# Kernel tuning notes

Hardware: AMD Instinct MI355X
Metric: run time of the kernel (lower is better)

The kernel has to match this reference:

```python
import jax, jax.numpy as jnp
import numpy as np

B, N, C, H = 4, 2048, 1024, 16
D = C // H  # head_dim = 64

def setup_inputs() -> dict:
    key = jax.random.key(0)
    k1, k2, k3, k4, k5, k6 = jax.random.split(key, 6)
    x = jax.random.normal(k1, (B, N, C), dtype=jnp.float32)
    rope_cos = jax.random.uniform(k2, (N, D), dtype=jnp.float32)
    rope_sin = jax.random.uniform(k3, (N, D), dtype=jnp.float32)
    w_qkv = jax.random.normal(k4, (3 * C, C), dtype=jnp.float32) * (C ** -0.5)
    w_proj = jax.random.normal(k5, (C, C), dtype=jnp.float32) * (C ** -0.5)
    b_proj = jax.random.normal(k6, (C,), dtype=jnp.float32) * 0.01
    return {"x": x, "rope_cos": rope_cos, "rope_sin": rope_sin,
            "w_qkv": w_qkv, "w_proj": w_proj, "b_proj": b_proj}

def _rotate_half(x):
    x1, x2 = jnp.split(x, 2, axis=-1)
    return jnp.concatenate((-x2, x1), axis=-1)

def _apply_rope(x, cos, sin):
    # x: [B,H,N,D]; cos/sin: [N,D] broadcast over B,H
    return x * cos + _rotate_half(x) * sin

def reference(x, rope_cos, rope_sin, w_qkv, w_proj, b_proj):
    Bc, Nc, Cc = x.shape
    scale = D ** -0.5
    qkv = jnp.einsum('bnc,fc->bnf', x, w_qkv)            # [B,N,3C]
    qkv = qkv.reshape(Bc, Nc, 3, H, D).transpose(2, 0, 3, 1, 4)  # [3,B,H,N,D]
    q, k, v = qkv[0], qkv[1], qkv[2]
    q = _apply_rope(q, rope_cos, rope_sin)
    k = _apply_rope(k, rope_cos, rope_sin)
    attn = jnp.einsum('bhnd,bhmd->bhnm', q, k) * scale   # [B,H,N,N]
    attn = jax.nn.softmax(attn, axis=-1)
    out = jnp.einsum('bhnm,bhmd->bhnd', attn, v)         # [B,H,N,D]
    out = out.transpose(0, 2, 1, 3).reshape(Bc, Nc, Cc)  # [B,N,C]
    return jnp.einsum('bnc,fc->bnf', out, w_proj) + b_proj
```

## Files before the change

### kernel.cpp

```cpp
#include <hip/hip_runtime.h>

#define MM   8192
#define CC   1024
#define F3   3072
#define NN   2048
#define HH   16
#define DD   64
#define QSCALE 0.1803368801111731f

typedef __attribute__((ext_vector_type(8))) __bf16 bf16x8;
typedef __attribute__((ext_vector_type(4))) float floatx4;
typedef __attribute__((ext_vector_type(4))) unsigned uintx4;

__device__ __forceinline__ unsigned short f2b(float f) {
  union { float f; unsigned int u; } v; v.f = f;
  unsigned int r = v.u + 0x7fffu + ((v.u >> 16) & 1u);
  return (unsigned short)(r >> 16);
}
__device__ __forceinline__ float b2f(unsigned short b) {
  union { unsigned int u; float f; } v; v.u = ((unsigned int)b) << 16;
  return v.f;
}

__device__ __forceinline__ void gl_lds16(const unsigned short* g, unsigned short* l) {
  __builtin_amdgcn_global_load_lds((const __attribute__((address_space(1))) void*)g,
                                   (__attribute__((address_space(3))) void*)l, 16, 0, 0);
}

__global__ __launch_bounds__(256) void cvt_all_k(const float* __restrict__ x,
                                                 const float* __restrict__ wqkv,
                                                 const float* __restrict__ wproj,
                                                 unsigned short* __restrict__ xb,
                                                 unsigned short* __restrict__ wqkvb,
                                                 unsigned short* __restrict__ wprojb) {
  const int N0 = MM * CC / 4, N1 = F3 * CC / 4, N2 = CC * CC / 4;
  const int total = N0 + N1 + N2;
  const int stride = (int)gridDim.x * 256;
  for (int i = blockIdx.x * 256 + threadIdx.x; i < total; i += stride) {
    const float* src;
    unsigned short* dst;
    int j;
    if (i < N0)            { src = x;     dst = xb;     j = i; }
    else if (i < N0 + N1)  { src = wqkv;  dst = wqkvb;  j = i - N0; }
    else                   { src = wproj; dst = wprojb; j = i - N0 - N1; }
    float4 v = ((const float4*)src)[j];
    ushort4 o;
    o.x = f2b(v.x); o.y = f2b(v.y); o.z = f2b(v.z); o.w = f2b(v.w);
    ((ushort4*)dst)[j] = o;
  }
}

template <int F, bool BF16OUT, bool ROPE>
__global__ __launch_bounds__(512, 2) void gemm_p(const unsigned short* __restrict__ A,
                                                 const unsigned short* __restrict__ Bm,
                                                 void* __restrict__ Cout,
                                                 const float* __restrict__ bias,
                                                 const float* __restrict__ rcp,
                                                 const float* __restrict__ spp, int K) {
  __shared__ alignas(16) unsigned short lA[3][128 * 64];
  __shared__ alignas(16) unsigned short lB[3][256 * 64];
  const int tid = threadIdx.x, lane = tid & 63, wave = tid >> 6;
  const int r16 = lane & 15, q4 = lane >> 4;
  const int wm = wave & 1, wn = wave >> 1;

  const int id = blockIdx.x;
  const int xcd = id & 7, slot = id >> 3;
  const int rx = xcd * 8 + (slot & 7), cy = slot >> 3;
  const int rowBase = rx * 128, colBase = cy * 256;

  const int cA0 = tid, cA1 = tid + 512;
  const int cB0 = tid, cB1 = tid + 512, cB2 = tid + 1024, cB3 = tid + 1536;
#define CHOFF(base, c) ((size_t)((base) + ((c) >> 3)) * K + ((((c) & 7) ^ (((c) >> 3) & 7)) << 3))
  const size_t aoff0 = CHOFF(rowBase, cA0), aoff1 = CHOFF(rowBase, cA1);
  const size_t boff0 = CHOFF(colBase, cB0), boff1 = CHOFF(colBase, cB1);
  const size_t boff2 = CHOFF(colBase, cB2), boff3 = CHOFF(colBase, cB3);
#undef CHOFF

#define STAGEP(kt, bsel) do { const int _k0 = (kt) * 64; \
    gl_lds16(A + aoff0 + _k0, &lA[bsel][cA0 * 8]); \
    gl_lds16(A + aoff1 + _k0, &lA[bsel][cA1 * 8]); \
    gl_lds16(Bm + boff0 + _k0, &lB[bsel][cB0 * 8]); \
    gl_lds16(Bm + boff1 + _k0, &lB[bsel][cB1 * 8]); \
    gl_lds16(Bm + boff2 + _k0, &lB[bsel][cB2 * 8]); \
    gl_lds16(Bm + boff3 + _k0, &lB[bsel][cB3 * 8]); } while (0)

  floatx4 acc[4][4];
  const floatx4 z = {0.f, 0.f, 0.f, 0.f};
#pragma unroll
  for (int i = 0; i < 4; ++i)
#pragma unroll
    for (int j = 0; j < 4; ++j) acc[i][j] = z;

  const int nt = K / 64;

  STAGEP(0, 0);
  STAGEP(1, 1);
  STAGEP(2, 2);
  asm volatile("s_waitcnt vmcnt(12)" ::: "memory");
  __builtin_amdgcn_s_barrier();
  __builtin_amdgcn_sched_barrier(0);

  int bs = 0;
  for (int t = 0; t < nt; ++t) {
    const unsigned short* la = &lA[bs][0];
    const unsigned short* lb = &lB[bs][0];
    bf16x8 af[4][2], bv[4][2];
#pragma unroll
    for (int im = 0; im < 4; ++im) {
      int row = wm * 64 + im * 16 + r16, r7 = row & 7;
      af[im][0] = *(const bf16x8*)(la + row * 64 + ((q4 ^ r7) << 3));
      af[im][1] = *(const bf16x8*)(la + row * 64 + (((4 + q4) ^ r7) << 3));
    }
#pragma unroll
    for (int jf = 0; jf < 4; ++jf) {
      int row = wn * 64 + jf * 16 + r16, r7 = row & 7;
      bv[jf][0] = *(const bf16x8*)(lb + row * 64 + ((q4 ^ r7) << 3));
      bv[jf][1] = *(const bf16x8*)(lb + row * 64 + (((4 + q4) ^ r7) << 3));
    }
    __builtin_amdgcn_s_setprio(1);
#pragma unroll
    for (int jf = 0; jf < 4; ++jf)
#pragma unroll
      for (int im = 0; im < 4; ++im) {
        acc[im][jf] = __builtin_amdgcn_mfma_f32_16x16x32_bf16(af[im][0], bv[jf][0], acc[im][jf], 0, 0, 0);
        acc[im][jf] = __builtin_amdgcn_mfma_f32_16x16x32_bf16(af[im][1], bv[jf][1], acc[im][jf], 0, 0, 0);
      }
    __builtin_amdgcn_s_setprio(0);

    __builtin_amdgcn_s_barrier();
    __builtin_amdgcn_sched_barrier(0);
    if (t + 3 < nt) {
      STAGEP(t + 3, bs);
      asm volatile("s_waitcnt vmcnt(12)" ::: "memory");
    } else {
      asm volatile("s_waitcnt vmcnt(0)" ::: "memory");
    }
    __builtin_amdgcn_sched_barrier(0);
    __builtin_amdgcn_s_barrier();
    __builtin_amdgcn_sched_barrier(0);
    bs = (bs == 2) ? 0 : bs + 1;
  }
#undef STAGEP

  if (ROPE) {
    int head = (colBase >> 6) + wn;
    if (head < 32) {
      const bool isq = head < 16;
#pragma unroll
      for (int im = 0; im < 4; ++im)
#pragma unroll
        for (int jf = 0; jf < 2; ++jf)
#pragma unroll
          for (int r = 0; r < 4; ++r) {
            int grow = rowBase + wm * 64 + im * 16 + q4 * 4 + r;
            int n = grow & (NN - 1);
            int dp = jf * 16 + r16;
            float x0 = acc[im][jf][r], x1 = acc[im][jf + 2][r];
            float c0 = rcp[n * DD + dp],      s0v = spp[n * DD + dp];
            float c1 = rcp[n * DD + dp + 32], s1v = spp[n * DD + dp + 32];
            float y0 = x0 * c0 - x1 * s0v;
            float y1 = x1 * c1 + x0 * s1v;
            if (isq) { y0 *= QSCALE; y1 *= QSCALE; }
            acc[im][jf][r] = y0;
            acc[im][jf + 2][r] = y1;
          }
    }
  }

#pragma unroll
  for (int im = 0; im < 4; ++im)
#pragma unroll
    for (int jf = 0; jf < 4; ++jf)
#pragma unroll
      for (int r = 0; r < 4; ++r) {
        int grow = rowBase + wm * 64 + im * 16 + q4 * 4 + r;
        int gcol = colBase + wn * 64 + jf * 16 + r16;
        if (BF16OUT)
          ((unsigned short*)Cout)[(size_t)grow * F + gcol] = f2b(acc[im][jf][r]);
        else
          ((float*)Cout)[(size_t)grow * F + gcol] = acc[im][jf][r] + bias[gcol];
      }
}

__global__ __launch_bounds__(256, 2) void attn_k(const unsigned short* __restrict__ qkv,
                                                 unsigned short* __restrict__ obuf) {
  __shared__ alignas(16) unsigned short sK[64 * 64];
  __shared__ alignas(16) unsigned short sVT[64 * 64];

  const int tid = threadIdx.x, lane = tid & 63, wave = tid >> 6;
  const int r16 = lane & 15, q4 = lane >> 4;

  const int id = blockIdx.x;
  const int xcd = id & 7, slot = id >> 3;
  const int bh = xcd * 8 + (slot >> 3);
  const int q0 = (slot & 7) * 256;
  const int b = bh >> 4, h = bh & 15;
  const unsigned short* qbase = qkv + (size_t)(b * NN) * F3 + h * DD;

  bf16x8 qf[4][2];
#pragma unroll
  for (int im = 0; im < 4; ++im)
#pragma unroll
    for (int kk = 0; kk < 2; ++kk)
      qf[im][kk] = *(const bf16x8*)(qbase +
          (size_t)(q0 + wave * 64 + im * 16 + r16) * F3 + kk * 32 + q4 * 8);

  const floatx4 z = {0.f, 0.f, 0.f, 0.f};
  floatx4 o[4][4];
  float lacc[4] = {0.f, 0.f, 0.f, 0.f};
#pragma unroll
  for (int im = 0; im < 4; ++im)
    for (int jd = 0; jd < 4; ++jd) o[im][jd] = z;

  const int krow0 = tid >> 3, kc8 = tid & 7;
  const int vkvp = tid >> 3, vc8 = tid & 7;
  const int mp = (vkvp & 16) | ((vkvp & 4) << 1) | ((vkvp & 2) << 1) |
                 ((vkvp & 8) >> 2) | (vkvp & 1);

  const unsigned short* kvb = qbase;
  int4 kreg0 = *(const int4*)(kvb + (size_t)krow0 * F3 + CC + kc8 * 8);
  int4 kreg1 = *(const int4*)(kvb + (size_t)(krow0 + 32) * F3 + CC + kc8 * 8);
  int4 vreg0 = *(const int4*)(kvb + (size_t)(2 * vkvp) * F3 + 2 * CC + vc8 * 8);
  int4 vreg1 = *(const int4*)(kvb + (size_t)(2 * vkvp + 1) * F3 + 2 * CC + vc8 * 8);

  for (int t = 0; t < NN / 64; ++t) {
    __syncthreads();

    *(int4*)(&sK[krow0 * 64 + ((kc8 ^ (krow0 & 7)) << 3)]) = kreg0;
    *(int4*)(&sK[(krow0 + 32) * 64 + ((kc8 ^ ((krow0 + 32) & 7)) << 3)]) = kreg1;
    {
      const unsigned* a0 = (const unsigned*)&vreg0;
      const unsigned* a1 = (const unsigned*)&vreg1;
#pragma unroll
      for (int w = 0; w < 4; ++w) {
        unsigned lo = __builtin_amdgcn_perm(a1[w], a0[w], 0x05040100u);
        unsigned hi = __builtin_amdgcn_perm(a1[w], a0[w], 0x07060302u);
        int d0 = vc8 * 8 + 2 * w;
        int sw0 = (2 * w + vc8) & 7;
        int sw1 = (2 * w + 1 + vc8) & 7;
        *(unsigned*)(&sVT[d0 * 64 + (((mp >> 2) ^ sw0) << 3) + 2 * (mp & 3)]) = lo;
        *(unsigned*)(&sVT[(d0 + 1) * 64 + (((mp >> 2) ^ sw1) << 3) + 2 * (mp & 3)]) = hi;
      }
    }

    if (t + 1 < NN / 64) {
      const unsigned short* nb = qkv + (size_t)(b * NN + (t + 1) * 64) * F3 + h * DD;
      kreg0 = *(const int4*)(nb + (size_t)krow0 * F3 + CC + kc8 * 8);
      kreg1 = *(const int4*)(nb + (size_t)(krow0 + 32) * F3 + CC + kc8 * 8);
      vreg0 = *(const int4*)(nb + (size_t)(2 * vkvp) * F3 + 2 * CC + vc8 * 8);
      vreg1 = *(const int4*)(nb + (size_t)(2 * vkvp + 1) * F3 + 2 * CC + vc8 * 8);
    }

    __syncthreads();

    floatx4 s[4][4];
    __builtin_amdgcn_s_setprio(1);
#pragma unroll
    for (int jn = 0; jn < 4; ++jn) {
      int row = jn * 16 + r16;
      bf16x8 kf0 = *(const bf16x8*)(&sK[row * 64 + ((q4 ^ (row & 7)) << 3)]);
      bf16x8 kf1 = *(const bf16x8*)(&sK[row * 64 + (((4 + q4) ^ (row & 7)) << 3)]);
#pragma unroll
      for (int im = 0; im < 4; ++im) {
        floatx4 a = z;
        a = __builtin_amdgcn_mfma_f32_16x16x32_bf16(kf0, qf[im][0], a, 0, 0, 0);
        a = __builtin_amdgcn_mfma_f32_16x16x32_bf16(kf1, qf[im][1], a, 0, 0, 0);
        s[im][jn] = a;
      }
    }
    __builtin_amdgcn_s_setprio(0);

    bf16x8 pf[4][2];
#pragma unroll
    for (int im = 0; im < 4; ++im) {
#pragma unroll
      for (int kk = 0; kk < 2; ++kk) {
        uintx4 pk;
#pragma unroll
        for (int j2 = 0; j2 < 2; ++j2) {
          int jn = 2 * kk + j2;
          float p0 = __builtin_amdgcn_exp2f(s[im][jn][0]);
          float p1 = __builtin_amdgcn_exp2f(s[im][jn][1]);
          float p2 = __builtin_amdgcn_exp2f(s[im][jn][2]);
          float p3 = __builtin_amdgcn_exp2f(s[im][jn][3]);
          lacc[im] += (p0 + p1) + (p2 + p3);
          asm("v_cvt_pk_bf16_f32 %0, %1, %2" : "=v"(pk[2 * j2]) : "v"(p0), "v"(p1));
          asm("v_cvt_pk_bf16_f32 %0, %1, %2" : "=v"(pk[2 * j2 + 1]) : "v"(p2), "v"(p3));
        }
        pf[im][kk] = __builtin_bit_cast(bf16x8, pk);
      }
    }

    __builtin_amdgcn_s_setprio(1);
#pragma unroll
    for (int jd = 0; jd < 4; ++jd) {
      int d = jd * 16 + r16;
      int swr = (d + (d >> 3)) & 7;
      bf16x8 vf0 = *(const bf16x8*)(&sVT[d * 64 + ((q4 ^ swr) << 3)]);
      bf16x8 vf1 = *(const bf16x8*)(&sVT[d * 64 + (((4 + q4) ^ swr) << 3)]);
#pragma unroll
      for (int im = 0; im < 4; ++im) {
        o[im][jd] = __builtin_amdgcn_mfma_f32_16x16x32_bf16(pf[im][0], vf0, o[im][jd], 0, 0, 0);
        o[im][jd] = __builtin_amdgcn_mfma_f32_16x16x32_bf16(pf[im][1], vf1, o[im][jd], 0, 0, 0);
      }
    }
    __builtin_amdgcn_s_setprio(0);
  }

#pragma unroll
  for (int im = 0; im < 4; ++im) {
    float l = lacc[im];
    l += __shfl_xor(l, 16);
    l += __shfl_xor(l, 32);
    float inv = 1.0f / l;
#pragma unroll
    for (int r = 0; r < 4; ++r) {
      float invr = __shfl(inv, q4 * 4 + r);
      int row = q0 + wave * 64 + im * 16 + q4 * 4 + r;
#pragma unroll
      for (int jd = 0; jd < 4; ++jd) {
        int col = h * DD + jd * 16 + r16;
        obuf[(size_t)(b * NN + row) * CC + col] = f2b(o[im][jd][r] * invr);
      }
    }
  }
}

extern "C" void kernel_launch(void* const* d_in, const int* in_sizes, int n_in,
                              void* d_out, int out_size, void* d_ws, size_t ws_size,
                              hipStream_t stream) {
  const float* x     = (const float*)d_in[0];
  const float* rc    = (const float*)d_in[1];
  const float* rs    = (const float*)d_in[2];
  const float* wqkv  = (const float*)d_in[3];
  const float* wproj = (const float*)d_in[4];
  const float* bproj = (const float*)d_in[5];
  float* out = (float*)d_out;

  char* w = (char*)d_ws;
  unsigned short* xb     = (unsigned short*)(w);
  unsigned short* wqkvb  = (unsigned short*)(w + 16777216);
  unsigned short* wprojb = (unsigned short*)(w + 23068672);
  unsigned short* qkvb   = (unsigned short*)(w + 25165824);
  unsigned short* obuf   = (unsigned short*)(w + 75497472);

  cvt_all_k<<<2048, 256, 0, stream>>>(x, wqkv, wproj, xb, wqkvb, wprojb);

  gemm_p<F3, true, true><<<768, 512, 0, stream>>>(
      xb, wqkvb, qkvb, nullptr, rc, rs, CC);

  attn_k<<<512, 256, 0, stream>>>(qkvb, obuf);

  gemm_p<CC, false, false><<<256, 512, 0, stream>>>(
      obuf, wprojb, out, bproj, nullptr, nullptr, CC);
}
```

Measured before the change: 263.5 us.

## Double-buffer K/V shared-memory tiles in attention loop to halve barriers

Shared-memory K and transposed V tiles are now double-buffered. Each iteration writes the next tile into the alternate buffer and issues global loads two tiles ahead, then computes on the current buffer. This cuts the two block barriers per iteration to one and lets LDS stores overlap compute. In exchange it doubles LDS use (32KB per block), which could affect occupancy at two blocks per CU.

```diff
diff --git a/kernel.cpp b/kernel.cpp
--- a/kernel.cpp
+++ b/kernel.cpp
@@ -184,8 +184,8 @@
 
 __global__ __launch_bounds__(256, 2) void attn_k(const unsigned short* __restrict__ qkv,
                                                  unsigned short* __restrict__ obuf) {
-  __shared__ alignas(16) unsigned short sK[64 * 64];
-  __shared__ alignas(16) unsigned short sVT[64 * 64];
+  __shared__ alignas(16) unsigned short sK[2][64 * 64];
+  __shared__ alignas(16) unsigned short sVT[2][64 * 64];
 
   const int tid = threadIdx.x, lane = tid & 63, wave = tid >> 6;
   const int r16 = lane & 15, q4 = lane >> 4;
@@ -217,18 +217,45 @@
   const int mp = (vkvp & 16) | ((vkvp & 4) << 1) | ((vkvp & 2) << 1) |
                  ((vkvp & 8) >> 2) | (vkvp & 1);
 
-  const unsigned short* kvb = qbase;
-  int4 kreg0 = *(const int4*)(kvb + (size_t)krow0 * F3 + CC + kc8 * 8);
-  int4 kreg1 = *(const int4*)(kvb + (size_t)(krow0 + 32) * F3 + CC + kc8 * 8);
-  int4 vreg0 = *(const int4*)(kvb + (size_t)(2 * vkvp) * F3 + 2 * CC + vc8 * 8);
-  int4 vreg1 = *(const int4*)(kvb + (size_t)(2 * vkvp + 1) * F3 + 2 * CC + vc8 * 8);
+  const int skoff0 = krow0 * 64 + ((kc8 ^ (krow0 & 7)) << 3);
+  const int skoff1 = (krow0 + 32) * 64 + ((kc8 ^ ((krow0 + 32) & 7)) << 3);
+
+  int4 kreg0 = *(const int4*)(qbase + (size_t)krow0 * F3 + CC + kc8 * 8);
+  int4 kreg1 = *(const int4*)(qbase + (size_t)(krow0 + 32) * F3 + CC + kc8 * 8);
+  int4 vreg0 = *(const int4*)(qbase + (size_t)(2 * vkvp) * F3 + 2 * CC + vc8 * 8);
+  int4 vreg1 = *(const int4*)(qbase + (size_t)(2 * vkvp + 1) * F3 + 2 * CC + vc8 * 8);
+
+  {
+    *(int4*)(&sK[0][skoff0]) = kreg0;
+    *(int4*)(&sK[0][skoff1]) = kreg1;
+    const unsigned* a0 = (const unsigned*)&vreg0;
+    const unsigned* a1 = (const unsigned*)&vreg1;
+#pragma unroll
+    for (int w = 0; w < 4; ++w) {
+      unsigned lo = __builtin_amdgcn_perm(a1[w], a0[w], 0x05040100u);
+      unsigned hi = __builtin_amdgcn_perm(a1[w], a0[w], 0x07060302u);
+      int d0 = vc8 * 8 + 2 * w;
+      int sw0 = (2 * w + vc8) & 7;
+      int sw1 = (2 * w + 1 + vc8) & 7;
+      *(unsigned*)(&sVT[0][d0 * 64 + (((mp >> 2) ^ sw0) << 3) + 2 * (mp & 3)]) = lo;
+      *(unsigned*)(&sVT[0][(d0 + 1) * 64 + (((mp >> 2) ^ sw1) << 3) + 2 * (mp & 3)]) = hi;
+    }
+  }
+  {
+    const unsigned short* nb = qbase + (size_t)64 * F3;
+    kreg0 = *(const int4*)(nb + (size_t)krow0 * F3 + CC + kc8 * 8);
+    kreg1 = *(const int4*)(nb + (size_t)(krow0 + 32) * F3 + CC + kc8 * 8);
+    vreg0 = *(const int4*)(nb + (size_t)(2 * vkvp) * F3 + 2 * CC + vc8 * 8);
+    vreg1 = *(const int4*)(nb + (size_t)(2 * vkvp + 1) * F3 + 2 * CC + vc8 * 8);
+  }
+  __syncthreads();
 
   for (int t = 0; t < NN / 64; ++t) {
-    __syncthreads();
-
-    *(int4*)(&sK[krow0 * 64 + ((kc8 ^ (krow0 & 7)) << 3)]) = kreg0;
-    *(int4*)(&sK[(krow0 + 32) * 64 + ((kc8 ^ ((krow0 + 32) & 7)) << 3)]) = kreg1;
-    {
+    const int p = t & 1;
+
+    if (t + 1 < NN / 64) {
+      *(int4*)(&sK[p ^ 1][skoff0]) = kreg0;
+      *(int4*)(&sK[p ^ 1][skoff1]) = kreg1;
       const unsigned* a0 = (const unsigned*)&vreg0;
       const unsigned* a1 = (const unsigned*)&vreg1;
 #pragma unroll
@@ -238,28 +265,25 @@
         int d0 = vc8 * 8 + 2 * w;
         int sw0 = (2 * w + vc8) & 7;
         int sw1 = (2 * w + 1 + vc8) & 7;
-        *(unsigned*)(&sVT[d0 * 64 + (((mp >> 2) ^ sw0) << 3) + 2 * (mp & 3)]) = lo;
-        *(unsigned*)(&sVT[(d0 + 1) * 64 + (((mp >> 2) ^ sw1) << 3) + 2 * (mp & 3)]) = hi;
-      }
-    }
-
-    if (t + 1 < NN / 64) {
-      const unsigned short* nb = qkv + (size_t)(b * NN + (t + 1) * 64) * F3 + h * DD;
-      kreg0 = *(const int4*)(nb + (size_t)krow0 * F3 + CC + kc8 * 8);
-      kreg1 = *(const int4*)(nb + (size_t)(krow0 + 32) * F3 + CC + kc8 * 8);
-      vreg0 = *(const int4*)(nb + (size_t)(2 * vkvp) * F3 + 2 * CC + vc8 * 8);
-      vreg1 = *(const int4*)(nb + (size_t)(2 * vkvp + 1) * F3 + 2 * CC + vc8 * 8);
-    }
-
-    __syncthreads();
+        *(unsigned*)(&sVT[p ^ 1][d0 * 64 + (((mp >> 2) ^ sw0) << 3) + 2 * (mp & 3)]) = lo;
+        *(unsigned*)(&sVT[p ^ 1][(d0 + 1) * 64 + (((mp >> 2) ^ sw1) << 3) + 2 * (mp & 3)]) = hi;
+      }
+      if (t + 2 < NN / 64) {
+        const unsigned short* nb = qbase + (size_t)((t + 2) * 64) * F3;
+        kreg0 = *(const int4*)(nb + (size_t)krow0 * F3 + CC + kc8 * 8);
+        kreg1 = *(const int4*)(nb + (size_t)(krow0 + 32) * F3 + CC + kc8 * 8);
+        vreg0 = *(const int4*)(nb + (size_t)(2 * vkvp) * F3 + 2 * CC + vc8 * 8);
+        vreg1 = *(const int4*)(nb + (size_t)(2 * vkvp + 1) * F3 + 2 * CC + vc8 * 8);
+      }
+    }
 
     floatx4 s[4][4];
     __builtin_amdgcn_s_setprio(1);
 #pragma unroll
     for (int jn = 0; jn < 4; ++jn) {
       int row = jn * 16 + r16;
-      bf16x8 kf0 = *(const bf16x8*)(&sK[row * 64 + ((q4 ^ (row & 7)) << 3)]);
-      bf16x8 kf1 = *(const bf16x8*)(&sK[row * 64 + (((4 + q4) ^ (row & 7)) << 3)]);
+      bf16x8 kf0 = *(const bf16x8*)(&sK[p][row * 64 + ((q4 ^ (row & 7)) << 3)]);
+      bf16x8 kf1 = *(const bf16x8*)(&sK[p][row * 64 + (((4 + q4) ^ (row & 7)) << 3)]);
 #pragma unroll
       for (int im = 0; im < 4; ++im) {
         floatx4 a = z;
@@ -296,8 +320,8 @@
     for (int jd = 0; jd < 4; ++jd) {
       int d = jd * 16 + r16;
       int swr = (d + (d >> 3)) & 7;
-      bf16x8 vf0 = *(const bf16x8*)(&sVT[d * 64 + ((q4 ^ swr) << 3)]);
-      bf16x8 vf1 = *(const bf16x8*)(&sVT[d * 64 + (((4 + q4) ^ swr) << 3)]);
+      bf16x8 vf0 = *(const bf16x8*)(&sVT[p][d * 64 + ((q4 ^ swr) << 3)]);
+      bf16x8 vf1 = *(const bf16x8*)(&sVT[p][d * 64 + (((4 + q4) ^ swr) << 3)]);
 #pragma unroll
       for (int im = 0; im < 4; ++im) {
         o[im][jd] = __builtin_amdgcn_mfma_f32_16x16x32_bf16(pf[im][0], vf0, o[im][jd], 0, 0, 0);
@@ -305,6 +329,8 @@
       }
     }
     __builtin_amdgcn_s_setprio(0);
+
+    __syncthreads();
   }
 
 #pragma unroll
```

Result: no change. 264.2 us (+0.3%).
